# Performance work log

Hardware: AMD Instinct MI355X
Metric: run time of the kernel (lower is better)

## Reference

```python
import jax, jax.numpy as jnp
import numpy as np

N_TOKENS, MODEL_DIM, NUM_EXPERTS = 65536, 1024, 64
CAPACITY_FACTOR = 1.0


def setup_inputs() -> dict:
    key = jax.random.key(0)
    k1, k2 = jax.random.split(key)
    x = jax.random.normal(k1, (N_TOKENS, MODEL_DIM), dtype=jnp.float32)
    # gate projection weight, torch Linear stores [out_features, in_features]
    wg = jax.random.normal(k2, (NUM_EXPERTS, MODEL_DIM), dtype=jnp.float32) * (1.0 / np.sqrt(MODEL_DIM))
    return {"x": x, "wg": wg}


def reference(x, wg):
    N, E = x.shape[0], wg.shape[0]
    logits = x @ wg.T                              # [N, E]
    # training-branch capacity: capacity_factor * ceil(N / E)
    capacity = int(CAPACITY_FACTOR * ((N + E - 1) // E))
    indices1_s = jnp.argmax(logits, axis=1)        # [N] top-1 expert per token
    gates = jax.nn.softmax(logits, axis=1)         # [N, E]
    mask1 = jax.nn.one_hot(indices1_s, E, dtype=gates.dtype)  # [N, E]
    gates1_s = jnp.sum(gates * mask1, axis=1)      # [N] gate value of chosen expert
    # locations1_s[i] = number of earlier tokens routed to the same expert
    # (exclusive prefix count = inclusive cumsum - 1 at the selected column)
    locations1 = jnp.cumsum(mask1, axis=0) - 1.0   # [N, E]
    locations1_s = jnp.sum(locations1 * mask1, axis=1).astype(jnp.int32)
    # auxiliary load-balance loss (float32 branch of the original)
    me = jnp.sum(gates, axis=0)                    # [E]
    ce = jnp.sum(mask1, axis=0)                    # [E]
    l_aux = jnp.sum(me * ce) * (E / (N * N))
    return (l_aux, indices1_s.astype(jnp.int32), capacity, locations1_s, gates1_s, E)
```

## Files before the change

kernel.cpp:

```cpp
#include <hip/hip_runtime.h>

#define NT 65536
#define MD 1024
#define NE 64
#define BK 32
#define NBLK (NT / 64)

#define SWZ(r, q) (((q) ^ (((r) >> 2) & 7)))

__global__ __launch_bounds__(256, 4) void gate_kernel(
    const float* __restrict__ x, const float* __restrict__ wg,
    float* __restrict__ out, unsigned* __restrict__ packed_ws,
    int* __restrict__ hist_ws, float* __restrict__ me)
{
    __shared__ __align__(16) float smem[2][128][32];

    const int tid = threadIdx.x;
    const int tx = tid & 15;
    const int ty = tid >> 4;
    const int t0 = blockIdx.x * 64;

    const int sr = tid >> 3;
    const int sq = tid & 7;
    const float* px0 = x  + (size_t)(t0 + sr) * MD + sq * 4;
    const float* px1 = px0 + (size_t)32 * MD;
    const float* pw0 = wg + (size_t)sr * MD + sq * 4;
    const float* pw1 = pw0 + (size_t)32 * MD;

    float4 g0 = *(const float4*)px0;
    float4 g1 = *(const float4*)px1;
    float4 g2 = *(const float4*)pw0;
    float4 g3 = *(const float4*)pw1;

#define STG(buf)                                                         \
    do {                                                                 \
        *(float4*)&smem[buf][sr      ][SWZ(sr,      sq) * 4] = g0;       \
        *(float4*)&smem[buf][sr + 32 ][SWZ(sr + 32, sq) * 4] = g1;       \
        *(float4*)&smem[buf][sr + 64 ][SWZ(sr + 64, sq) * 4] = g2;       \
        *(float4*)&smem[buf][sr + 96 ][SWZ(sr + 96, sq) * 4] = g3;       \
    } while (0)

    STG(0);
    __syncthreads();

    float acc[4][4];
#pragma unroll
    for (int i = 0; i < 4; ++i)
#pragma unroll
        for (int j = 0; j < 4; ++j) acc[i][j] = 0.f;

    for (int it = 0; it < MD / BK; ++it) {
        const int cur = it & 1;
        if (it < MD / BK - 1) {
            const int kn = (it + 1) * BK;
            g0 = *(const float4*)(px0 + kn);
            g1 = *(const float4*)(px1 + kn);
            g2 = *(const float4*)(pw0 + kn);
            g3 = *(const float4*)(pw1 + kn);
        }
#pragma unroll
        for (int q = 0; q < 8; ++q) {
            float4 A[4], B[4];
#pragma unroll
            for (int i = 0; i < 4; ++i)
                A[i] = *(const float4*)&smem[cur][ty * 4 + i][SWZ(ty * 4 + i, q) * 4];
#pragma unroll
            for (int j = 0; j < 4; ++j)
                B[j] = *(const float4*)&smem[cur][64 + tx * 4 + j][SWZ(64 + tx * 4 + j, q) * 4];
#pragma unroll
            for (int i = 0; i < 4; ++i)
#pragma unroll
                for (int j = 0; j < 4; ++j) {
                    acc[i][j] = fmaf(A[i].x, B[j].x, acc[i][j]);
                    acc[i][j] = fmaf(A[i].y, B[j].y, acc[i][j]);
                    acc[i][j] = fmaf(A[i].z, B[j].z, acc[i][j]);
                    acc[i][j] = fmaf(A[i].w, B[j].w, acc[i][j]);
                }
        }
        if (it < MD / BK - 1) STG(cur ^ 1);
        __syncthreads();
    }

    float* lt  = &smem[0][0][0];
    float* inv = lt + 4160;

#pragma unroll
    for (int i = 0; i < 4; ++i)
#pragma unroll
        for (int j = 0; j < 4; ++j)
            lt[(ty * 4 + i) * 65 + tx * 4 + j] = acc[i][j];
    __syncthreads();

    if (tid < 64) {
        const int t = tid;
        float m = -1e30f; int am = 0;
        for (int e = 0; e < NE; ++e) {
            float v = lt[t * 65 + e];
            if (v > m) { m = v; am = e; }
        }
        float s = 0.f;
        for (int e = 0; e < NE; ++e) {
            float ev = __expf(lt[t * 65 + e] - m);
            lt[t * 65 + e] = ev;
            s += ev;
        }
        float g = 1.0f / s;
        const int gt = t0 + t;
        out[1 + gt] = (float)am;
        out[2 + 2 * NT + gt] = g;
        inv[t] = g;

        const unsigned long long below = (1ull << t) - 1ull;
        int rank = 0, mycnt = 0;
        for (int e = 0; e < NE; ++e) {
            unsigned long long msk = __ballot(am == e);
            if (t == e)  mycnt = (int)__popcll(msk);
            if (am == e) rank  = (int)__popcll(msk & below);
        }
        packed_ws[gt] = (unsigned)am | ((unsigned)rank << 8);
        hist_ws[blockIdx.x * NE + t] = mycnt;
    }
    __syncthreads();

    if (tid < NE) {
        const int e = tid;
        float s = 0.f;
        for (int t = 0; t < 64; ++t) s += lt[t * 65 + e] * inv[t];
        atomicAdd(&me[e], s);
    }
}

__global__ __launch_bounds__(256) void scan_kernel(
    int* __restrict__ hist_ws, float* __restrict__ ce)
{
    const int e = blockIdx.x;
    const int tid = threadIdx.x;
    const int lane = tid & 63, wave = tid >> 6;
    __shared__ int wtot[4];

    int h[4];
#pragma unroll
    for (int j = 0; j < 4; ++j) h[j] = hist_ws[(tid * 4 + j) * NE + e];
    int s = h[0] + h[1] + h[2] + h[3];

    int scan = s;
#pragma unroll
    for (int d = 1; d < 64; d <<= 1) {
        int o = __shfl_up(scan, d, 64);
        if (lane >= d) scan += o;
    }
    if (lane == 63) wtot[wave] = scan;
    __syncthreads();
    int wpre = 0;
#pragma unroll
    for (int w = 0; w < 4; ++w)
        if (w < wave) wpre += wtot[w];

    int run = wpre + scan - s;
#pragma unroll
    for (int j = 0; j < 4; ++j) {
        hist_ws[(tid * 4 + j) * NE + e] = run;
        run += h[j];
    }
    if (tid == 255) ce[e] = (float)run;
}

__global__ __launch_bounds__(256) void emit_kernel(
    const unsigned* __restrict__ packed_ws, const int* __restrict__ offs_ws,
    float* __restrict__ out)
{
    const int i = blockIdx.x * 256 + threadIdx.x;
    const unsigned p = packed_ws[i];
    const int am = (int)(p & 63u);
    const int rank = (int)(p >> 8);
    const int b = i >> 6;
    out[2 + NT + i] = (float)(offs_ws[b * NE + am] + rank);
}

__global__ void finalize_kernel(const float* __restrict__ me,
                                const float* __restrict__ ce,
                                float* __restrict__ out)
{
    int tid = threadIdx.x;
    float v = me[tid] * ce[tid];
#pragma unroll
    for (int d = 32; d > 0; d >>= 1) v += __shfl_down(v, d, 64);
    if (tid == 0) {
        out[0] = v * (float)((double)NE / ((double)NT * (double)NT));
        out[1 + NT] = 1024.0f;
        out[2 + 3 * NT] = 64.0f;
    }
}

extern "C" void kernel_launch(void* const* d_in, const int* in_sizes, int n_in,
                              void* d_out, int out_size, void* d_ws, size_t ws_size,
                              hipStream_t stream)
{
    const float* x  = (const float*)d_in[0];
    const float* wg = (const float*)d_in[1];
    float* out = (float*)d_out;

    unsigned* packed_ws = (unsigned*)d_ws;
    int* hist_ws = (int*)((char*)d_ws + (size_t)NT * 4);
    float* me = (float*)((char*)d_ws + (size_t)NT * 4 + (size_t)NBLK * NE * 4);
    float* ce = me + NE;

    hipMemsetAsync(me, 0, NE * sizeof(float), stream);
    gate_kernel<<<NBLK, 256, 0, stream>>>(x, wg, out, packed_ws, hist_ws, me);
    scan_kernel<<<NE, 256, 0, stream>>>(hist_ws, ce);
    emit_kernel<<<NT / 256, 256, 0, stream>>>(packed_ws, hist_ws, out);
    finalize_kernel<<<1, 64, 0, stream>>>(me, ce, out);
}
```

Measured before the change: 424.3 us.

## Compute gate logits with split-bf16 MFMA and fp32 rescue for near-ties

Replaces the fp32 FMA tiled GEMM with MFMA 16x16x32 bf16, emulating fp32 with a hi/lo split (three MFMAs per tile). The weight split is done by a small pre-kernel, and the activation split happens on the fly. Tokens whose top-two logits are within 0.01 are flagged and recomputed in exact fp32 by a rescue kernel, so argmax and gate stay correct. Rank and histogram computation moves into a separate kernel. This adds launches and approximation risk, and the softmax sums feeding the load-balance term still come from the approximate logits.

```diff
diff --git a/kernel.cpp b/kernel.cpp
--- a/kernel.cpp
+++ b/kernel.cpp
@@ -1,102 +1,104 @@
 #include <hip/hip_runtime.h>
+#include <hip/hip_bf16.h>
 
 #define NT 65536
 #define MD 1024
 #define NE 64
-#define BK 32
-#define NBLK (NT / 64)
-
-#define SWZ(r, q) (((q) ^ (((r) >> 2) & 7)))
-
-__global__ __launch_bounds__(256, 4) void gate_kernel(
-    const float* __restrict__ x, const float* __restrict__ wg,
-    float* __restrict__ out, unsigned* __restrict__ packed_ws,
-    int* __restrict__ hist_ws, float* __restrict__ me)
-{
-    __shared__ __align__(16) float smem[2][128][32];
-
+
+typedef __attribute__((ext_vector_type(8))) short s8v;
+typedef __attribute__((ext_vector_type(4))) float f4v;
+
+static __device__ inline short bf16bits(float v) {
+    __hip_bfloat16 b = __float2bfloat16(v);
+    return *reinterpret_cast<short*>(&b);
+}
+static __device__ inline float bf16tof(short s) {
+    return __uint_as_float(((unsigned)(unsigned short)s) << 16);
+}
+
+__global__ __launch_bounds__(256) void wsplit_kernel(
+    const float* __restrict__ wg, short* __restrict__ wgh, short* __restrict__ wgl)
+{
+    const int gid = blockIdx.x * 256 + threadIdx.x;
+    const int lane = gid & 63;
+    const int tile = (gid >> 6) & 3;
+    const int kc = gid >> 8;
+    const int n = tile * 16 + (lane & 15);
+    const int k0 = kc * 32 + (lane >> 4) * 8;
+    const float* src = wg + (size_t)n * MD + k0;
+    short h[8], l[8];
+#pragma unroll
+    for (int j = 0; j < 8; ++j) {
+        float v = src[j];
+        short hb = bf16bits(v);
+        h[j] = hb;
+        l[j] = bf16bits(v - bf16tof(hb));
+    }
+    s8v hv, lv;
+#pragma unroll
+    for (int j = 0; j < 8; ++j) { hv[j] = h[j]; lv[j] = l[j]; }
+    *(s8v*)(wgh + (size_t)gid * 8) = hv;
+    *(s8v*)(wgl + (size_t)gid * 8) = lv;
+}
+
+__global__ __launch_bounds__(256) void gate_mfma(
+    const float* __restrict__ x, const short* __restrict__ wgh,
+    const short* __restrict__ wgl, float* __restrict__ out,
+    unsigned char* __restrict__ am8, unsigned char* __restrict__ flag,
+    float* __restrict__ me)
+{
+    __shared__ float lt[64 * 65 + 64];
     const int tid = threadIdx.x;
-    const int tx = tid & 15;
-    const int ty = tid >> 4;
+    const int lane = tid & 63;
+    const int wv = tid >> 6;
     const int t0 = blockIdx.x * 64;
 
-    const int sr = tid >> 3;
-    const int sq = tid & 7;
-    const float* px0 = x  + (size_t)(t0 + sr) * MD + sq * 4;
-    const float* px1 = px0 + (size_t)32 * MD;
-    const float* pw0 = wg + (size_t)sr * MD + sq * 4;
-    const float* pw1 = pw0 + (size_t)32 * MD;
-
-    float4 g0 = *(const float4*)px0;
-    float4 g1 = *(const float4*)px1;
-    float4 g2 = *(const float4*)pw0;
-    float4 g3 = *(const float4*)pw1;
-
-#define STG(buf)                                                         \
-    do {                                                                 \
-        *(float4*)&smem[buf][sr      ][SWZ(sr,      sq) * 4] = g0;       \
-        *(float4*)&smem[buf][sr + 32 ][SWZ(sr + 32, sq) * 4] = g1;       \
-        *(float4*)&smem[buf][sr + 64 ][SWZ(sr + 64, sq) * 4] = g2;       \
-        *(float4*)&smem[buf][sr + 96 ][SWZ(sr + 96, sq) * 4] = g3;       \
-    } while (0)
-
-    STG(0);
-    __syncthreads();
-
-    float acc[4][4];
-#pragma unroll
-    for (int i = 0; i < 4; ++i)
-#pragma unroll
-        for (int j = 0; j < 4; ++j) acc[i][j] = 0.f;
-
-    for (int it = 0; it < MD / BK; ++it) {
-        const int cur = it & 1;
-        if (it < MD / BK - 1) {
-            const int kn = (it + 1) * BK;
-            g0 = *(const float4*)(px0 + kn);
-            g1 = *(const float4*)(px1 + kn);
-            g2 = *(const float4*)(pw0 + kn);
-            g3 = *(const float4*)(pw1 + kn);
-        }
-#pragma unroll
-        for (int q = 0; q < 8; ++q) {
-            float4 A[4], B[4];
-#pragma unroll
-            for (int i = 0; i < 4; ++i)
-                A[i] = *(const float4*)&smem[cur][ty * 4 + i][SWZ(ty * 4 + i, q) * 4];
-#pragma unroll
-            for (int j = 0; j < 4; ++j)
-                B[j] = *(const float4*)&smem[cur][64 + tx * 4 + j][SWZ(64 + tx * 4 + j, q) * 4];
-#pragma unroll
-            for (int i = 0; i < 4; ++i)
-#pragma unroll
-                for (int j = 0; j < 4; ++j) {
-                    acc[i][j] = fmaf(A[i].x, B[j].x, acc[i][j]);
-                    acc[i][j] = fmaf(A[i].y, B[j].y, acc[i][j]);
-                    acc[i][j] = fmaf(A[i].z, B[j].z, acc[i][j]);
-                    acc[i][j] = fmaf(A[i].w, B[j].w, acc[i][j]);
-                }
-        }
-        if (it < MD / BK - 1) STG(cur ^ 1);
-        __syncthreads();
-    }
-
-    float* lt  = &smem[0][0][0];
+    const int arow = t0 + wv * 16 + (lane & 15);
+    const float* xr = x + (size_t)arow * MD + (lane >> 4) * 8;
+    const short* bh_base = wgh + lane * 8;
+    const short* bl_base = wgl + lane * 8;
+
+    f4v acc[4] = {f4v{0,0,0,0}, f4v{0,0,0,0}, f4v{0,0,0,0}, f4v{0,0,0,0}};
+
+#pragma unroll 2
+    for (int kc = 0; kc < 32; ++kc) {
+        float4 a0 = *(const float4*)(xr + kc * 32);
+        float4 a1 = *(const float4*)(xr + kc * 32 + 4);
+        float av[8] = {a0.x, a0.y, a0.z, a0.w, a1.x, a1.y, a1.z, a1.w};
+        s8v ah, al;
+#pragma unroll
+        for (int j = 0; j < 8; ++j) {
+            short hb = bf16bits(av[j]);
+            ah[j] = hb;
+            al[j] = bf16bits(av[j] - bf16tof(hb));
+        }
+        const short* bp = bh_base + (size_t)kc * 2048;
+        const short* lp = bl_base + (size_t)kc * 2048;
+#pragma unroll
+        for (int t = 0; t < 4; ++t) {
+            s8v bh = *(const s8v*)(bp + t * 512);
+            s8v bl = *(const s8v*)(lp + t * 512);
+            acc[t] = __builtin_amdgcn_mfma_f32_16x16x32_bf16(ah, bh, acc[t], 0, 0, 0);
+            acc[t] = __builtin_amdgcn_mfma_f32_16x16x32_bf16(al, bh, acc[t], 0, 0, 0);
+            acc[t] = __builtin_amdgcn_mfma_f32_16x16x32_bf16(ah, bl, acc[t], 0, 0, 0);
+        }
+    }
+
+#pragma unroll
+    for (int t = 0; t < 4; ++t)
+#pragma unroll
+        for (int r = 0; r < 4; ++r)
+            lt[(wv * 16 + (lane >> 4) * 4 + r) * 65 + t * 16 + (lane & 15)] = acc[t][r];
+    __syncthreads();
+
     float* inv = lt + 4160;
-
-#pragma unroll
-    for (int i = 0; i < 4; ++i)
-#pragma unroll
-        for (int j = 0; j < 4; ++j)
-            lt[(ty * 4 + i) * 65 + tx * 4 + j] = acc[i][j];
-    __syncthreads();
-
     if (tid < 64) {
         const int t = tid;
-        float m = -1e30f; int am = 0;
+        float m = -1e30f, m2 = -1e30f; int am = 0;
         for (int e = 0; e < NE; ++e) {
             float v = lt[t * 65 + e];
-            if (v > m) { m = v; am = e; }
+            if (v > m) { m2 = m; m = v; am = e; }
+            else if (v > m2) m2 = v;
         }
         float s = 0.f;
         for (int e = 0; e < NE; ++e) {
@@ -106,19 +108,10 @@
         }
         float g = 1.0f / s;
         const int gt = t0 + t;
-        out[1 + gt] = (float)am;
         out[2 + 2 * NT + gt] = g;
+        am8[gt] = (unsigned char)am;
+        flag[gt] = (m - m2 < 0.01f) ? 1 : 0;
         inv[t] = g;
-
-        const unsigned long long below = (1ull << t) - 1ull;
-        int rank = 0, mycnt = 0;
-        for (int e = 0; e < NE; ++e) {
-            unsigned long long msk = __ballot(am == e);
-            if (t == e)  mycnt = (int)__popcll(msk);
-            if (am == e) rank  = (int)__popcll(msk & below);
-        }
-        packed_ws[gt] = (unsigned)am | ((unsigned)rank << 8);
-        hist_ws[blockIdx.x * NE + t] = mycnt;
     }
     __syncthreads();
 
@@ -130,6 +123,70 @@
     }
 }
 
+__global__ __launch_bounds__(256) void rescue_kernel(
+    const float* __restrict__ x, const float* __restrict__ wg,
+    const unsigned char* __restrict__ flag, unsigned char* __restrict__ am8,
+    float* __restrict__ out)
+{
+    __shared__ float part[256];
+    __shared__ float lg[64];
+    __shared__ int list[256];
+    __shared__ int cnt;
+    const int tid = threadIdx.x;
+    const int base = blockIdx.x * 256;
+
+    if (tid == 0) cnt = 0;
+    __syncthreads();
+    if (flag[base + tid]) { int p = atomicAdd(&cnt, 1); list[p] = base + tid; }
+    __syncthreads();
+    const int n = cnt;
+
+    const int e = tid & 63, c = tid >> 6;
+    for (int i = 0; i < n; ++i) {
+        const int t = list[i];
+        const float4* xr = (const float4*)(x + (size_t)t * MD + c * 256);
+        const float4* wr = (const float4*)(wg + (size_t)e * MD + c * 256);
+        float s = 0.f;
+#pragma unroll 4
+        for (int j = 0; j < 64; ++j) {
+            float4 xa = xr[j], wa = wr[j];
+            s += xa.x * wa.x + xa.y * wa.y + xa.z * wa.z + xa.w * wa.w;
+        }
+        part[tid] = s;
+        __syncthreads();
+        if (tid < 64) lg[tid] = part[tid] + part[tid + 64] + part[tid + 128] + part[tid + 192];
+        __syncthreads();
+        if (tid == 0) {
+            float m = -1e30f; int am = 0;
+            for (int q = 0; q < NE; ++q) { float v = lg[q]; if (v > m) { m = v; am = q; } }
+            float ssum = 0.f;
+            for (int q = 0; q < NE; ++q) ssum += __expf(lg[q] - m);
+            am8[t] = (unsigned char)am;
+            out[2 + 2 * NT + t] = 1.0f / ssum;
+        }
+        __syncthreads();
+    }
+}
+
+__global__ __launch_bounds__(256) void rankhist_kernel(
+    const unsigned char* __restrict__ am8, float* __restrict__ out,
+    unsigned* __restrict__ packed, int* __restrict__ hist)
+{
+    const int t = blockIdx.x * 256 + threadIdx.x;
+    const int lane = t & 63;
+    const int am = am8[t];
+    out[1 + t] = (float)am;
+    const unsigned long long below = (1ull << lane) - 1ull;
+    int rank = 0, mycnt = 0;
+    for (int e = 0; e < NE; ++e) {
+        unsigned long long msk = __ballot(am == e);
+        if (lane == e) mycnt = (int)__popcll(msk);
+        if (am == e)   rank  = (int)__popcll(msk & below);
+    }
+    packed[t] = (unsigned)am | ((unsigned)rank << 8);
+    hist[(t >> 6) * NE + lane] = mycnt;
+}
+
 __global__ __launch_bounds__(256) void scan_kernel(
     int* __restrict__ hist_ws, float* __restrict__ ce)
 {
@@ -166,15 +223,14 @@
 }
 
 __global__ __launch_bounds__(256) void emit_kernel(
-    const unsigned* __restrict__ packed_ws, const int* __restrict__ offs_ws,
+    const unsigned* __restrict__ packed, const int* __restrict__ offs,
     float* __restrict__ out)
 {
     const int i = blockIdx.x * 256 + threadIdx.x;
-    const unsigned p = packed_ws[i];
+    const unsigned p = packed[i];
     const int am = (int)(p & 63u);
     const int rank = (int)(p >> 8);
-    const int b = i >> 6;
-    out[2 + NT + i] = (float)(offs_ws[b * NE + am] + rank);
+    out[2 + NT + i] = (float)(offs[(i >> 6) * NE + am] + rank);
 }
 
 __global__ void finalize_kernel(const float* __restrict__ me,
@@ -200,14 +256,22 @@
     const float* wg = (const float*)d_in[1];
     float* out = (float*)d_out;
 
-    unsigned* packed_ws = (unsigned*)d_ws;
-    int* hist_ws = (int*)((char*)d_ws + (size_t)NT * 4);
-    float* me = (float*)((char*)d_ws + (size_t)NT * 4 + (size_t)NBLK * NE * 4);
+    char* ws = (char*)d_ws;
+    short* wgh = (short*)ws;
+    short* wgl = (short*)(ws + 131072);
+    unsigned char* am8  = (unsigned char*)(ws + 262144);
+    unsigned char* flag = (unsigned char*)(ws + 327680);
+    unsigned* packed = (unsigned*)(ws + 393216);
+    int* hist = (int*)(ws + 655360);
+    float* me = (float*)(ws + 917504);
     float* ce = me + NE;
 
     hipMemsetAsync(me, 0, NE * sizeof(float), stream);
-    gate_kernel<<<NBLK, 256, 0, stream>>>(x, wg, out, packed_ws, hist_ws, me);
-    scan_kernel<<<NE, 256, 0, stream>>>(hist_ws, ce);
-    emit_kernel<<<NT / 256, 256, 0, stream>>>(packed_ws, hist_ws, out);
+    wsplit_kernel<<<32, 256, 0, stream>>>(wg, wgh, wgl);
+    gate_mfma<<<NT / 64, 256, 0, stream>>>(x, wgh, wgl, out, am8, flag, me);
+    rescue_kernel<<<NT / 256, 256, 0, stream>>>(x, wg, flag, am8, out);
+    rankhist_kernel<<<NT / 256, 256, 0, stream>>>(am8, out, packed, hist);
+    scan_kernel<<<NE, 256, 0, stream>>>(hist, ce);
+    emit_kernel<<<NT / 256, 256, 0, stream>>>(packed, hist, out);
     finalize_kernel<<<1, 64, 0, stream>>>(me, ce, out);
 }
```

Result: slower. 589.7 us (+39.0%).
